# Kernel optimization log

Hardware: AMD Instinct MI355X
Metric: run time of the kernel (lower is better)

Reference implementation:

```python
import jax, jax.numpy as jnp
import numpy as np

ALPHA = float(np.exp(-0.1))  # leak factor exp(-dt/tau) with dt/tau = 0.1


def setup_inputs() -> dict:
    key = jax.random.key(0)
    k1, k2 = jax.random.split(key)
    B, T, H, O = 128, 512, 1024, 256
    x = jax.random.normal(k1, (B, T, H), dtype=jnp.float32)
    # xavier_uniform init for (H, O) weight
    limit = float(np.sqrt(6.0 / (H + O)))
    weight_end = jax.random.uniform(k2, (H, O), dtype=jnp.float32,
                                    minval=-limit, maxval=limit)
    return {"x": x, "weight_end": weight_end}


def reference(x, weight_end):
    # x: [B, T, H], weight_end: [H, O]
    h2 = jnp.einsum('bth,ho->bto', x, weight_end)  # [B, T, O]
    B, T, O = h2.shape
    # leaky-integrate scan over first T-1 steps, accumulating softmax(mem)
    h_seq = jnp.swapaxes(h2[:, :T - 1, :], 0, 1)  # [T-1, B, O]

    def step(carry, h_t):
        mem, out = carry
        mem = ALPHA * mem + (1.0 - ALPHA) * h_t
        out = out + jax.nn.softmax(mem, axis=-1)
        return (mem, out), None

    init = (jnp.zeros((B, O), h2.dtype), jnp.zeros((B, O), h2.dtype))
    (_, out), _ = jax.lax.scan(step, init, h_seq)
    return out
```

## Files before the change

### kernel.cpp

```cpp
#include <hip/hip_runtime.h>

#define B_DIM 128
#define T_DIM 512
#define H_DIM 1024
#define O_DIM 256

typedef short bf16x8 __attribute__((ext_vector_type(8)));
typedef float f32x4 __attribute__((ext_vector_type(4)));

__device__ __forceinline__ unsigned short f2bf(float f) {
    union { float f; unsigned u; } v; v.f = f;
    unsigned u = v.u;
    u += 0x7fffu + ((u >> 16) & 1u);
    return (unsigned short)(u >> 16);
}

__device__ __forceinline__ unsigned tpk(float a, float b) {
    union { float f; unsigned u; } x{a}, y{b};
    return __builtin_amdgcn_perm(y.u, x.u, 0x07060302u);
}

__device__ __forceinline__ void async16(const void* g, void* l) {
    __builtin_amdgcn_global_load_lds(
        (const __attribute__((address_space(1))) unsigned int*)g,
        (__attribute__((address_space(3))) unsigned int*)l, 16, 0, 0);
}

__global__ __launch_bounds__(256) void transpose_w(const float* __restrict__ W,
                                                   unsigned short* __restrict__ Wt) {
    __shared__ float tile[32][33];
    int h0 = blockIdx.x * 32;
    int o0 = blockIdx.y * 32;
    int tx = threadIdx.x;
    int ty = threadIdx.y;
#pragma unroll
    for (int j = 0; j < 32; j += 8)
        tile[ty + j][tx] = W[(size_t)(h0 + ty + j) * O_DIM + o0 + tx];
    __syncthreads();
#pragma unroll
    for (int j = 0; j < 32; j += 8)
        Wt[(size_t)(o0 + ty + j) * H_DIM + h0 + tx] = f2bf(tile[tx][ty + j]);
}

__global__ __launch_bounds__(256) void gemm_bf16(const float* __restrict__ x,
                                                 const unsigned short* __restrict__ Wt,
                                                 unsigned short* __restrict__ h2) {
    __shared__ __align__(16) unsigned short As[128 * 40];
    __shared__ __align__(16) unsigned short Bs[4 * 128 * 8];

    const int tid  = threadIdx.x;
    const int mb   = blockIdx.x >> 1;
    const int nb   = blockIdx.x & 1;
    const int m0   = mb * 128, n0 = nb * 128;
    const int r    = tid >> 1;
    const int hh   = tid & 1;
    const int lane = tid & 63;
    const int wave = tid >> 6;
    const int wm   = wave >> 1, wn = wave & 1;
    const int rowsel = lane & 15, quad = lane >> 4;

    const float* xg = x + (size_t)(m0 + r) * H_DIM + hh * 16;
    uint4* awp = (uint4*)&As[r * 40 + hh * 16];

    const unsigned short* wg0 = Wt + (size_t)(n0 + lane) * H_DIM + wave * 8;
    const unsigned short* wg1 = wg0 + (size_t)64 * H_DIM;
    unsigned short* bs0 = &Bs[wave * 1024];
    unsigned short* bs1 = &Bs[wave * 1024 + 512];

    const unsigned short* afp = &As[(wm * 64 + rowsel) * 40 + quad * 8];
    const unsigned short* bfp = &Bs[quad * 1024 + (wn * 64 + rowsel) * 8];

    f32x4 acc[4][4];
#pragma unroll
    for (int i = 0; i < 4; ++i)
#pragma unroll
        for (int j = 0; j < 4; ++j)
            acc[i][j] = (f32x4){0.f, 0.f, 0.f, 0.f};

    for (int k0 = 0; k0 < H_DIM; k0 += 32) {
        async16(wg0, bs0);
        async16(wg1, bs1);

        const float4* xa = (const float4*)xg;
        float4 a0 = xa[0], a1 = xa[1], a2 = xa[2], a3 = xa[3];
        uint4 p0, p1;
        p0.x = tpk(a0.x, a0.y); p0.y = tpk(a0.z, a0.w);
        p0.z = tpk(a1.x, a1.y); p0.w = tpk(a1.z, a1.w);
        p1.x = tpk(a2.x, a2.y); p1.y = tpk(a2.z, a2.w);
        p1.z = tpk(a3.x, a3.y); p1.w = tpk(a3.z, a3.w);
        awp[0] = p0;  awp[1] = p1;
        __syncthreads();

        bf16x8 af[4], bfr[4];
#pragma unroll
        for (int i = 0; i < 4; ++i) {
            af[i]  = *(const bf16x8*)(afp + i * 16 * 40);
            bfr[i] = *(const bf16x8*)(bfp + i * 16 * 8);
        }
#pragma unroll
        for (int i = 0; i < 4; ++i)
#pragma unroll
            for (int j = 0; j < 4; ++j)
                acc[i][j] = __builtin_amdgcn_mfma_f32_16x16x32_bf16(af[i], bfr[j], acc[i][j], 0, 0, 0);
        __syncthreads();

        xg += 32;
        wg0 += 32;
        wg1 += 32;
    }

#pragma unroll
    for (int i = 0; i < 4; ++i) {
#pragma unroll
        for (int j = 0; j < 4; ++j) {
            int gm = m0 + wm * 64 + i * 16 + quad * 4;
            int gn = n0 + wn * 64 + j * 16 + rowsel;
            unsigned short* cp = h2 + (size_t)gm * O_DIM + gn;
            cp[0 * O_DIM] = f2bf(acc[i][j][0]);
            cp[1 * O_DIM] = f2bf(acc[i][j][1]);
            cp[2 * O_DIM] = f2bf(acc[i][j][2]);
            cp[3 * O_DIM] = f2bf(acc[i][j][3]);
        }
    }
}

__global__ __launch_bounds__(64) void snn_scan(const unsigned short* __restrict__ h2,
                                               float* __restrict__ out) {
    const int b = blockIdx.x >> 3;
    const int c = blockIdx.x & 7;
    const int t_start = c * 64;
    const int t_end   = min(t_start + 64, T_DIM - 1);
    const int s0      = max(0, t_start - 64);
    const int lane    = threadIdx.x;

    const float A   = 0.90483741803595957f;
    const float OMA = 0.09516258196404043f;

    const unsigned short* base = h2 + (size_t)b * T_DIM * O_DIM + lane * 4;
#define LD(row) (*(const uint2*)(base + (size_t)(row) * O_DIM))

    float4 mem = {0.f, 0.f, 0.f, 0.f};
    float4 acc = {0.f, 0.f, 0.f, 0.f};

    uint2 u0 = LD(s0), u1 = LD(s0 + 1), u2 = LD(s0 + 2), u3 = LD(s0 + 3);

    const int nIter = (t_end - s0 + 3) & ~3;

#define STEP(U, T)                                                              \
    {                                                                           \
        union { unsigned u; float f; } l0, h0, l1, h1;                          \
        l0.u = (U).x << 16; h0.u = (U).x & 0xffff0000u;                         \
        l1.u = (U).y << 16; h1.u = (U).y & 0xffff0000u;                         \
        mem.x = A * mem.x + OMA * l0.f;                                         \
        mem.y = A * mem.y + OMA * h0.f;                                         \
        mem.z = A * mem.z + OMA * l1.f;                                         \
        mem.w = A * mem.w + OMA * h1.f;                                         \
        if ((T) >= t_start && (T) < t_end) {                                    \
            float e0 = __expf(mem.x), e1 = __expf(mem.y);                       \
            float e2 = __expf(mem.z), e3 = __expf(mem.w);                       \
            float s = e0 + e1 + e2 + e3;                                        \
            s += __shfl_xor(s, 1);                                              \
            s += __shfl_xor(s, 2);                                              \
            s += __shfl_xor(s, 4);                                              \
            s += __shfl_xor(s, 8);                                              \
            s += __shfl_xor(s, 16);                                             \
            s += __shfl_xor(s, 32);                                             \
            float inv = 1.0f / s;                                               \
            acc.x += e0 * inv; acc.y += e1 * inv;                               \
            acc.z += e2 * inv; acc.w += e3 * inv;                               \
        }                                                                       \
    }

    for (int t = s0; t < s0 + nIter; t += 4) {
        STEP(u0, t);     u0 = LD(min(t + 4, T_DIM - 1));
        STEP(u1, t + 1); u1 = LD(min(t + 5, T_DIM - 1));
        STEP(u2, t + 2); u2 = LD(min(t + 6, T_DIM - 1));
        STEP(u3, t + 3); u3 = LD(min(t + 7, T_DIM - 1));
    }
#undef STEP
#undef LD

    float* op = out + b * O_DIM + lane * 4;
    atomicAdd(op + 0, acc.x);
    atomicAdd(op + 1, acc.y);
    atomicAdd(op + 2, acc.z);
    atomicAdd(op + 3, acc.w);
}

extern "C" void kernel_launch(void* const* d_in, const int* in_sizes, int n_in,
                              void* d_out, int out_size, void* d_ws, size_t ws_size,
                              hipStream_t stream) {
    const float* x = (const float*)d_in[0];
    const float* W = (const float*)d_in[1];
    float* out = (float*)d_out;

    unsigned short* h2 = (unsigned short*)d_ws;
    unsigned short* Wt = (unsigned short*)((char*)d_ws +
                         (size_t)B_DIM * T_DIM * O_DIM * sizeof(unsigned short));

    hipMemsetAsync(d_out, 0, (size_t)B_DIM * O_DIM * sizeof(float), stream);
    transpose_w<<<dim3(H_DIM / 32, O_DIM / 32), dim3(32, 8), 0, stream>>>(W, Wt);
    gemm_bf16<<<dim3((B_DIM * T_DIM / 128) * 2), 256, 0, stream>>>(x, Wt, h2);
    snn_scan<<<dim3(B_DIM * 8), 64, 0, stream>>>(h2, out);
}
```

Before: 464.9 us.

## Double-buffer GEMM LDS tiles and prefetch next K-slice during MFMA

Converts the bf16 GEMM main loop to a double-buffered LDS scheme. The next K-slice of x (fp32 loads) and W (async global-to-LDS) is issued before the current slice's MFMAs, and the converted A tile is written to the other buffer afterwards, so only one barrier per iteration is needed. The A-load mapping is also changed so each lane reads 4 rows of 16 bytes, and launch bounds now request 4 blocks per CU. The goal is to hide global load latency behind compute, at the cost of twice the LDS and more registers holding prefetched data.

```diff
diff --git a/kernel.cpp b/kernel.cpp
--- a/kernel.cpp
+++ b/kernel.cpp
@@ -42,33 +42,28 @@
         Wt[(size_t)(o0 + ty + j) * H_DIM + h0 + tx] = f2bf(tile[tx][ty + j]);
 }
 
-__global__ __launch_bounds__(256) void gemm_bf16(const float* __restrict__ x,
-                                                 const unsigned short* __restrict__ Wt,
-                                                 unsigned short* __restrict__ h2) {
-    __shared__ __align__(16) unsigned short As[128 * 40];
-    __shared__ __align__(16) unsigned short Bs[4 * 128 * 8];
+__global__ __launch_bounds__(256, 4) void gemm_bf16(const float* __restrict__ x,
+                                                    const unsigned short* __restrict__ Wt,
+                                                    unsigned short* __restrict__ h2) {
+    __shared__ __align__(16) unsigned short As[2][128 * 40];
+    __shared__ __align__(16) unsigned short Bs[2][4 * 128 * 8];
 
     const int tid  = threadIdx.x;
     const int mb   = blockIdx.x >> 1;
     const int nb   = blockIdx.x & 1;
     const int m0   = mb * 128, n0 = nb * 128;
-    const int r    = tid >> 1;
-    const int hh   = tid & 1;
     const int lane = tid & 63;
     const int wave = tid >> 6;
     const int wm   = wave >> 1, wn = wave & 1;
     const int rowsel = lane & 15, quad = lane >> 4;
 
-    const float* xg = x + (size_t)(m0 + r) * H_DIM + hh * 16;
-    uint4* awp = (uint4*)&As[r * 40 + hh * 16];
+    const int arow = wave * 32 + (lane >> 3);
+    const int akf  = (lane & 7) * 4;
+    const float* ag = x + (size_t)(m0 + arow) * H_DIM + akf;
+    const int aoff = arow * 40 + akf;
 
     const unsigned short* wg0 = Wt + (size_t)(n0 + lane) * H_DIM + wave * 8;
     const unsigned short* wg1 = wg0 + (size_t)64 * H_DIM;
-    unsigned short* bs0 = &Bs[wave * 1024];
-    unsigned short* bs1 = &Bs[wave * 1024 + 512];
-
-    const unsigned short* afp = &As[(wm * 64 + rowsel) * 40 + quad * 8];
-    const unsigned short* bfp = &Bs[quad * 1024 + (wn * 64 + rowsel) * 8];
 
     f32x4 acc[4][4];
 #pragma unroll
@@ -77,36 +72,57 @@
         for (int j = 0; j < 4; ++j)
             acc[i][j] = (f32x4){0.f, 0.f, 0.f, 0.f};
 
-    for (int k0 = 0; k0 < H_DIM; k0 += 32) {
-        async16(wg0, bs0);
-        async16(wg1, bs1);
-
-        const float4* xa = (const float4*)xg;
-        float4 a0 = xa[0], a1 = xa[1], a2 = xa[2], a3 = xa[3];
-        uint4 p0, p1;
-        p0.x = tpk(a0.x, a0.y); p0.y = tpk(a0.z, a0.w);
-        p0.z = tpk(a1.x, a1.y); p0.w = tpk(a1.z, a1.w);
-        p1.x = tpk(a2.x, a2.y); p1.y = tpk(a2.z, a2.w);
-        p1.z = tpk(a3.x, a3.y); p1.w = tpk(a3.z, a3.w);
-        awp[0] = p0;  awp[1] = p1;
+    {
+        float4 a[4];
+#pragma unroll
+        for (int i = 0; i < 4; ++i)
+            a[i] = *(const float4*)(ag + (size_t)i * 8 * H_DIM);
+        async16(wg0, &Bs[0][wave * 1024]);
+        async16(wg1, &Bs[0][wave * 1024 + 512]);
+#pragma unroll
+        for (int i = 0; i < 4; ++i) {
+            uint2 p;
+            p.x = tpk(a[i].x, a[i].y);
+            p.y = tpk(a[i].z, a[i].w);
+            *(uint2*)&As[0][aoff + i * 8 * 40] = p;
+        }
+    }
+
+    for (int k = 0; k < 32; ++k) {
+        const int cur = k & 1, nxt = cur ^ 1;
         __syncthreads();
 
+        float4 a[4];
+        if (k + 1 < 32) {
+            const float* agk = ag + (size_t)(k + 1) * 32;
+#pragma unroll
+            for (int i = 0; i < 4; ++i)
+                a[i] = *(const float4*)(agk + (size_t)i * 8 * H_DIM);
+            async16(wg0 + (size_t)(k + 1) * 32, &Bs[nxt][wave * 1024]);
+            async16(wg1 + (size_t)(k + 1) * 32, &Bs[nxt][wave * 1024 + 512]);
+        }
+
         bf16x8 af[4], bfr[4];
 #pragma unroll
         for (int i = 0; i < 4; ++i) {
-            af[i]  = *(const bf16x8*)(afp + i * 16 * 40);
-            bfr[i] = *(const bf16x8*)(bfp + i * 16 * 8);
+            af[i]  = *(const bf16x8*)&As[cur][(wm * 64 + rowsel + i * 16) * 40 + quad * 8];
+            bfr[i] = *(const bf16x8*)&Bs[cur][quad * 1024 + (wn * 64 + rowsel + i * 16) * 8];
         }
 #pragma unroll
         for (int i = 0; i < 4; ++i)
 #pragma unroll
             for (int j = 0; j < 4; ++j)
                 acc[i][j] = __builtin_amdgcn_mfma_f32_16x16x32_bf16(af[i], bfr[j], acc[i][j], 0, 0, 0);
-        __syncthreads();
-
-        xg += 32;
-        wg0 += 32;
-        wg1 += 32;
+
+        if (k + 1 < 32) {
+#pragma unroll
+            for (int i = 0; i < 4; ++i) {
+                uint2 p;
+                p.x = tpk(a[i].x, a[i].y);
+                p.y = tpk(a[i].z, a[i].w);
+                *(uint2*)&As[nxt][aoff + i * 8 * 40] = p;
+            }
+        }
     }
 
 #pragma unroll
```

Result: faster. 455.7 us (-2.0%).
